# Kernel tuning notes

Measured on AMD Instinct MI355X. Metric: run time of the kernel, lower is better.

The kernel has to match this reference:

```python
import jax, jax.numpy as jnp
import numpy as np

N_NODES = 50000
N_EDGES = 600000
NODE_DIM = 128
HIDDEN = 128
LN_EPS = 1e-5


def setup_inputs() -> dict:
    key = jax.random.key(0)
    ks = jax.random.split(key, 12)
    x = jax.random.normal(ks[0], (N_NODES, NODE_DIM), dtype=jnp.float32)
    edge_index = jax.random.randint(ks[1], (2, N_EDGES), 0, N_NODES, dtype=jnp.int32)
    # GCNConv weights (glorot-ish scaling)
    W1 = jax.random.normal(ks[2], (NODE_DIM, HIDDEN), dtype=jnp.float32) / np.sqrt(NODE_DIM)
    b1 = jnp.zeros((HIDDEN,), jnp.float32)
    W2 = jax.random.normal(ks[3], (HIDDEN, HIDDEN), dtype=jnp.float32) / np.sqrt(HIDDEN)
    b2 = jnp.zeros((HIDDEN,), jnp.float32)
    g1 = jnp.ones((HIDDEN,), jnp.float32)
    beta1 = jnp.zeros((HIDDEN,), jnp.float32)
    g2 = jnp.ones((HIDDEN,), jnp.float32)
    beta2 = jnp.zeros((HIDDEN,), jnp.float32)
    return {"x": x, "edge_index": edge_index, "W1": W1, "b1": b1, "g1": g1,
            "beta1": beta1, "W2": W2, "b2": b2, "g2": g2, "beta2": beta2}


def _gcn_conv(x, src, dst, norm, W, b, n):
    # x' = sum_{j->i} norm_ji * (x_j @ W) + b   (self-loops already in src/dst)
    h = x @ W                                   # [N, H]
    msg = h[src] * norm[:, None]                # [E+N, H]
    out = jax.ops.segment_sum(msg, dst, num_segments=n)
    return out + b


def _layer_norm(x, gamma, beta):
    mu = jnp.mean(x, axis=-1, keepdims=True)
    var = jnp.mean((x - mu) ** 2, axis=-1, keepdims=True)
    return (x - mu) * jax.lax.rsqrt(var + LN_EPS) * gamma + beta


def reference(x, edge_index, W1, b1, g1, beta1, W2, b2, g2, beta2):
    n = x.shape[0]
    loop = jnp.arange(n, dtype=edge_index.dtype)
    src = jnp.concatenate([edge_index[0], loop])
    dst = jnp.concatenate([edge_index[1], loop])
    # symmetric normalization with self-loops (PyG GCNConv default)
    deg = jax.ops.segment_sum(jnp.ones_like(dst, dtype=x.dtype), dst, num_segments=n)
    dinv = jnp.where(deg > 0, jax.lax.rsqrt(jnp.maximum(deg, 1.0)), 0.0)
    norm = dinv[src] * dinv[dst]                # [E+N]

    h = _gcn_conv(x, src, dst, norm, W1, b1, n)
    h = _layer_norm(h, g1, beta1)
    h = jax.nn.relu(h)                          # relu between layers only
    h = _gcn_conv(h, src, dst, norm, W2, b2, n)
    h = _layer_norm(h, g2, beta2)
    return h
```

## Files before the change

### kernel.cpp

```cpp
#include <hip/hip_runtime.h>

#define DIM 128
#define LN_EPS 1e-5f

typedef __attribute__((ext_vector_type(8))) short bf16x8;
typedef __attribute__((ext_vector_type(4))) float f32x4;

static __device__ __forceinline__ unsigned short f2bf(float f) {
    unsigned int u = __builtin_bit_cast(unsigned int, f);
    u += 0x7fffu + ((u >> 16) & 1u);
    return (unsigned short)(u >> 16);
}
static __device__ __forceinline__ float bf2f_lo(unsigned int u) {
    return __builtin_bit_cast(float, u << 16);
}
static __device__ __forceinline__ float bf2f_hi(unsigned int u) {
    return __builtin_bit_cast(float, u & 0xffff0000u);
}

__global__ __launch_bounds__(256) void cvt_count_kernel(const float* __restrict__ X,
                                                        unsigned short* __restrict__ Y, int n4,
                                                        int nx4b,
                                                        const float* __restrict__ W1,
                                                        const float* __restrict__ W2,
                                                        unsigned short* __restrict__ Wt1,
                                                        unsigned short* __restrict__ Wt2,
                                                        const int* __restrict__ dst,
                                                        int* __restrict__ counts, int E) {
    int b = blockIdx.x;
    if (b < nx4b) {
        int i = b * 256 + threadIdx.x;
        if (i < n4) {
            float4 v = ((const float4*)X)[i];
            ushort4 o;
            o.x = f2bf(v.x); o.y = f2bf(v.y); o.z = f2bf(v.z); o.w = f2bf(v.w);
            ((ushort4*)Y)[i] = o;
        }
    } else if (b < nx4b + 128) {
        int elem = (b - nx4b) * 256 + threadIdx.x;
        int which = elem >> 14;
        int rest = elem & 16383;
        int c = rest >> 7;
        int k = rest & 127;
        const float* W = which ? W2 : W1;
        unsigned short* Wt = which ? Wt2 : Wt1;
        Wt[c * 128 + k] = f2bf(W[k * 128 + c]);
    } else {
        int e = (b - nx4b - 128) * 256 + threadIdx.x;
        if (e < E) atomicAdd(&counts[dst[e]], 1);
    }
}

__global__ __launch_bounds__(256) void scan1_kernel(const int* __restrict__ counts,
                                                    int* __restrict__ tmp,
                                                    int* __restrict__ bsums,
                                                    float* __restrict__ dinv, int n) {
    __shared__ int ts[256];
    int tid = threadIdx.x;
    int base = blockIdx.x * 1024 + tid * 4;
    int v[4];
#pragma unroll
    for (int j = 0; j < 4; ++j) {
        int i = base + j;
        v[j] = (i < n) ? counts[i] : 0;
        if (i < n) dinv[i] = rsqrtf((float)(v[j] + 1));
    }
    int s = v[0] + v[1] + v[2] + v[3];
    ts[tid] = s;
    __syncthreads();
    for (int off = 1; off < 256; off <<= 1) {
        int t2 = (tid >= off) ? ts[tid - off] : 0;
        __syncthreads();
        ts[tid] += t2;
        __syncthreads();
    }
    int excl = ts[tid] - s;
    int pre = excl;
#pragma unroll
    for (int j = 0; j < 4; ++j) {
        int i = base + j;
        if (i < n) tmp[i] = pre;
        pre += v[j];
    }
    if (tid == 255) bsums[blockIdx.x] = ts[255];
}

__global__ __launch_bounds__(256) void scan3_kernel(const int* __restrict__ tmp,
                                                    const int* __restrict__ bsums,
                                                    int* __restrict__ rowptr,
                                                    int* __restrict__ cursor,
                                                    int n, int E, int nb) {
    __shared__ int s_add;
    if (threadIdx.x < 64) {
        int lane = threadIdx.x;
        int v = (lane < nb) ? bsums[lane] : 0;
        int x = v;
#pragma unroll
        for (int off = 1; off < 64; off <<= 1) {
            int y = __shfl_up(x, off);
            if (lane >= off) x += y;
        }
        int excl = x - v;
        int mine = __builtin_amdgcn_readlane(excl, blockIdx.x);
        if (lane == 0) s_add = mine;
    }
    __syncthreads();
    int add = s_add;
    int base = blockIdx.x * 1024 + threadIdx.x * 4;
#pragma unroll
    for (int j = 0; j < 4; ++j) {
        int i = base + j;
        if (i < n) {
            int val = tmp[i] + add;
            rowptr[i] = val;
            cursor[i] = val;
        }
    }
    if (blockIdx.x == 0 && threadIdx.x == 0) rowptr[n] = E;
}

__global__ __launch_bounds__(256) void fill_kernel(const int* __restrict__ src,
                                                   const int* __restrict__ dst,
                                                   int* __restrict__ cursor,
                                                   unsigned short* __restrict__ colsrc, int E) {
    int e = blockIdx.x * 256 + threadIdx.x;
    if (e < E) {
        int p = atomicAdd(&cursor[dst[e]], 1);
        colsrc[p] = (unsigned short)src[e];
    }
}

__global__ __launch_bounds__(256) void gemm_mfma_kernel(const unsigned short* __restrict__ A,
                                                        const unsigned short* __restrict__ Bt,
                                                        const float* __restrict__ dinv,
                                                        unsigned short* __restrict__ H,
                                                        int n, int ntiles) {
    __shared__ unsigned short Wlds[128 * 136];

    for (int u = threadIdx.x; u < 2048; u += 256) {
        int row = u >> 4;
        int sub = u & 15;
        *(bf16x8*)&Wlds[row * 136 + sub * 8] = *(const bf16x8*)(Bt + row * 128 + sub * 8);
    }
    __syncthreads();

    int wid = threadIdx.x >> 6;
    int lane = threadIdx.x & 63;
    int tile = blockIdx.x * 4 + wid;
    if (tile >= ntiles) tile = ntiles - 1;
    int r0 = tile * 16;
    int mrow = lane & 15;
    int kgrp = lane >> 4;

    int arow_i = r0 + mrow;
    if (arow_i > n - 1) arow_i = n - 1;
    const unsigned short* arow = A + (size_t)arow_i * DIM + kgrp * 8;

    f32x4 acc[8];
#pragma unroll
    for (int t = 0; t < 8; ++t) acc[t] = (f32x4){0.f, 0.f, 0.f, 0.f};

#pragma unroll
    for (int kc = 0; kc < 4; ++kc) {
        bf16x8 af = *(const bf16x8*)(arow + kc * 32);
#pragma unroll
        for (int t = 0; t < 8; ++t) {
            bf16x8 bfv = *(const bf16x8*)&Wlds[(t * 16 + mrow) * 136 + kc * 32 + kgrp * 8];
            acc[t] = __builtin_amdgcn_mfma_f32_16x16x32_bf16(af, bfv, acc[t], 0, 0, 0);
        }
    }

    float dv[4];
#pragma unroll
    for (int reg = 0; reg < 4; ++reg) {
        int rr = r0 + kgrp * 4 + reg;
        dv[reg] = (rr < n) ? dinv[rr] : 0.f;
    }
#pragma unroll
    for (int t = 0; t < 8; ++t) {
#pragma unroll
        for (int reg = 0; reg < 4; ++reg) {
            int row = r0 + kgrp * 4 + reg;
            if (row < n) {
                int col = t * 16 + mrow;
                H[(size_t)row * DIM + col] = f2bf(acc[t][reg] * dv[reg]);
            }
        }
    }
}

__global__ __launch_bounds__(256) void gather_ln_kernel(const int* __restrict__ rowptr,
                                                        const unsigned short* __restrict__ colsrc,
                                                        const unsigned int* __restrict__ Hb,
                                                        const float* __restrict__ dinv,
                                                        const float* __restrict__ bias,
                                                        const float* __restrict__ gamma,
                                                        const float* __restrict__ beta,
                                                        unsigned int* __restrict__ out_bf,
                                                        float* __restrict__ out_f,
                                                        int n, int relu) {
    int wid = threadIdx.x >> 6;
    int lane = threadIdx.x & 63;
    int r = blockIdx.x * 4 + wid;
    if (r >= n) return;

    float di = dinv[r];
    float2 bb = ((const float2*)bias)[lane];
    float2 gg = ((const float2*)gamma)[lane];
    float2 be = ((const float2*)beta)[lane];

    unsigned int su = Hb[(size_t)r * 64 + lane];
    float ax = bf2f_lo(su), ay = bf2f_hi(su);

    int p = rowptr[r];
    int p1 = rowptr[r + 1];
    while (p < p1) {
        int cnt = p1 - p;
        if (cnt > 16) cnt = 16;
        int gi = p + lane;
        gi = gi < p1 ? gi : p1 - 1;
        int idxv = (int)colsrc[gi];

        unsigned int h[16];
#pragma unroll
        for (int j = 0; j < 16; ++j) {
            int s = __builtin_amdgcn_readlane(idxv, j);
            h[j] = Hb[(size_t)s * 64 + lane];
        }

#pragma unroll
        for (int j = 0; j < 16; ++j) {
            bool act = (j < cnt);
            ax += act ? bf2f_lo(h[j]) : 0.f;
            ay += act ? bf2f_hi(h[j]) : 0.f;
        }
        p += cnt;
    }

    float vx = ax * di + bb.x;
    float vy = ay * di + bb.y;

    float s1 = vx + vy;
    float s2 = vx * vx + vy * vy;
#pragma unroll
    for (int off = 32; off > 0; off >>= 1) {
        s1 += __shfl_xor(s1, off);
        s2 += __shfl_xor(s2, off);
    }
    float mu = s1 * (1.f / 128.f);
    float var = s2 * (1.f / 128.f) - mu * mu;
    float rstd = rsqrtf(var + LN_EPS);

    float ox = (vx - mu) * rstd * gg.x + be.x;
    float oy = (vy - mu) * rstd * gg.y + be.y;
    if (relu) {
        ox = fmaxf(ox, 0.f);
        oy = fmaxf(oy, 0.f);
    }
    if (out_bf) {
        unsigned int pk = (unsigned int)f2bf(ox) | ((unsigned int)f2bf(oy) << 16);
        out_bf[(size_t)r * 64 + lane] = pk;
    } else {
        ((float2*)out_f)[(size_t)r * 64 + lane] = make_float2(ox, oy);
    }
}

extern "C" void kernel_launch(void* const* d_in, const int* in_sizes, int n_in,
                              void* d_out, int out_size, void* d_ws, size_t ws_size,
                              hipStream_t stream) {
    const float* x   = (const float*)d_in[0];
    const int*   ei  = (const int*)d_in[1];
    const float* W1  = (const float*)d_in[2];
    const float* b1  = (const float*)d_in[3];
    const float* g1  = (const float*)d_in[4];
    const float* be1 = (const float*)d_in[5];
    const float* W2  = (const float*)d_in[6];
    const float* b2  = (const float*)d_in[7];
    const float* g2  = (const float*)d_in[8];
    const float* be2 = (const float*)d_in[9];

    int n = in_sizes[0] / DIM;
    int E = in_sizes[1] / 2;
    const int* src = ei;
    const int* dst = ei + E;

    char* wp = (char*)d_ws;
    auto alloc = [&](size_t bytes) {
        void* p = (void*)wp;
        wp += (bytes + 255) & ~(size_t)255;
        return p;
    };
    float*          dinv   = (float*)alloc((size_t)n * 4);
    int*            counts = (int*)alloc((size_t)n * 4);
    int*            tmp    = (int*)alloc((size_t)n * 4);
    int*            rowptr = (int*)alloc((size_t)(n + 1) * 4);
    int*            cursor = (int*)alloc((size_t)n * 4);
    int*            bsums  = (int*)alloc(64 * 4);
    unsigned short* colsrc = (unsigned short*)alloc((size_t)E * 2);
    unsigned short* xb     = (unsigned short*)alloc((size_t)n * DIM * 2);
    unsigned short* Wt1    = (unsigned short*)alloc(128 * 128 * 2);
    unsigned short* Wt2    = (unsigned short*)alloc(128 * 128 * 2);
    unsigned short* H      = (unsigned short*)alloc((size_t)n * DIM * 2);
    unsigned short* Y1     = (unsigned short*)alloc((size_t)n * DIM * 2);

    hipMemsetAsync(counts, 0, (size_t)n * 4, stream);

    int n4 = n * DIM / 4;
    int nx4b = (n4 + 255) / 256;
    int gE = (E + 255) / 256;
    cvt_count_kernel<<<nx4b + 128 + gE, 256, 0, stream>>>(x, xb, n4, nx4b, W1, W2, Wt1, Wt2,
                                                          dst, counts, E);

    int nb1 = (n + 1023) / 1024;
    scan1_kernel<<<nb1, 256, 0, stream>>>(counts, tmp, bsums, dinv, n);
    scan3_kernel<<<nb1, 256, 0, stream>>>(tmp, bsums, rowptr, cursor, n, E, nb1);
    fill_kernel<<<gE, 256, 0, stream>>>(src, dst, cursor, colsrc, E);

    int ntiles = (n + 15) / 16;
    int gG = (ntiles + 3) / 4;
    int gA = (n + 3) / 4;

    gemm_mfma_kernel<<<gG, 256, 0, stream>>>(xb, Wt1, dinv, H, n, ntiles);
    gather_ln_kernel<<<gA, 256, 0, stream>>>(rowptr, colsrc, (const unsigned int*)H, dinv,
                                             b1, g1, be1, (unsigned int*)Y1, nullptr, n, 1);

    gemm_mfma_kernel<<<gG, 256, 0, stream>>>(Y1, Wt2, dinv, H, n, ntiles);
    gather_ln_kernel<<<gA, 256, 0, stream>>>(rowptr, colsrc, (const unsigned int*)H, dinv,
                                             b2, g2, be2, nullptr, (float*)d_out, n, 0);
}
```

Before: 235.7 us.

## Split feature dim into four column slabs for cache-local gather, separate LayerNorm

The GEMM now writes H in a slab layout of four 32-column quarters, each stored contiguously. A new gather kernel aggregates one quarter per block, with the quarter chosen by block index, so each gather pass touches a 3.2 MB slab that can stay in L2 or LLC instead of the full 12.8 MB feature matrix. Aggregates are written as bf16 to a new buffer, and a separate LayerNorm kernel reads them back. This adds one kernel launch per layer, an extra round trip through memory, and an extra bf16 rounding of the aggregated sums before LayerNorm.

```diff
diff --git a/kernel.cpp b/kernel.cpp
--- a/kernel.cpp
+++ b/kernel.cpp
@@ -178,67 +178,90 @@
     }
 #pragma unroll
     for (int t = 0; t < 8; ++t) {
+        int q = t >> 1;
+        int c = (t & 1) * 16 + mrow;
 #pragma unroll
         for (int reg = 0; reg < 4; ++reg) {
             int row = r0 + kgrp * 4 + reg;
             if (row < n) {
-                int col = t * 16 + mrow;
-                H[(size_t)row * DIM + col] = f2bf(acc[t][reg] * dv[reg]);
+                H[((size_t)q * n + row) * 32 + c] = f2bf(acc[t][reg] * dv[reg]);
             }
         }
     }
 }
 
-__global__ __launch_bounds__(256) void gather_ln_kernel(const int* __restrict__ rowptr,
-                                                        const unsigned short* __restrict__ colsrc,
-                                                        const unsigned int* __restrict__ Hb,
-                                                        const float* __restrict__ dinv,
-                                                        const float* __restrict__ bias,
-                                                        const float* __restrict__ gamma,
-                                                        const float* __restrict__ beta,
-                                                        unsigned int* __restrict__ out_bf,
-                                                        float* __restrict__ out_f,
-                                                        int n, int relu) {
+__global__ __launch_bounds__(256) void gatherq_kernel(const int* __restrict__ rowptr,
+                                                      const unsigned short* __restrict__ colsrc,
+                                                      const unsigned int* __restrict__ H32,
+                                                      unsigned int* __restrict__ agg32,
+                                                      int n) {
+    int b = blockIdx.x;
+    int q = (b & 7) >> 1;
+    int i = (b >> 3) * 2 + (b & 1);
+    int wid = threadIdx.x >> 6;
+    int lane = threadIdx.x & 63;
+    int g = lane >> 4;
+    int t = lane & 15;
+    int r = i * 16 + wid * 4 + g;
+    if (r >= n) return;
+
+    const unsigned int* Hq = H32 + (size_t)q * n * 16;
+
+    unsigned int hv = Hq[(size_t)r * 16 + t];
+    float ax = bf2f_lo(hv), ay = bf2f_hi(hv);
+
+    int p = rowptr[r];
+    int p1 = rowptr[r + 1];
+    int gbase = g << 4;
+    while (p < p1) {
+        int cnt = p1 - p;
+        if (cnt > 16) cnt = 16;
+        int gi = p + t;
+        gi = gi < p1 ? gi : p1 - 1;
+        int idxv = (int)colsrc[gi];
+
+        unsigned int h[16];
+#pragma unroll
+        for (int j = 0; j < 16; ++j) {
+            int s = __shfl(idxv, gbase + j);
+            h[j] = Hq[(size_t)s * 16 + t];
+        }
+#pragma unroll
+        for (int j = 0; j < 16; ++j) {
+            bool act = (j < cnt);
+            ax += act ? bf2f_lo(h[j]) : 0.f;
+            ay += act ? bf2f_hi(h[j]) : 0.f;
+        }
+        p += cnt;
+    }
+
+    unsigned int pk = (unsigned int)f2bf(ax) | ((unsigned int)f2bf(ay) << 16);
+    __builtin_nontemporal_store(pk, &agg32[((size_t)q * n + r) * 16 + t]);
+}
+
+__global__ __launch_bounds__(256) void ln_kernel(const unsigned int* __restrict__ agg32,
+                                                 const float* __restrict__ dinv,
+                                                 const float* __restrict__ bias,
+                                                 const float* __restrict__ gamma,
+                                                 const float* __restrict__ beta,
+                                                 unsigned int* __restrict__ out_bf,
+                                                 float* __restrict__ out_f,
+                                                 int n, int relu) {
     int wid = threadIdx.x >> 6;
     int lane = threadIdx.x & 63;
     int r = blockIdx.x * 4 + wid;
     if (r >= n) return;
+    int q = lane >> 4;
+    int t = lane & 15;
 
     float di = dinv[r];
     float2 bb = ((const float2*)bias)[lane];
     float2 gg = ((const float2*)gamma)[lane];
     float2 be = ((const float2*)beta)[lane];
 
-    unsigned int su = Hb[(size_t)r * 64 + lane];
-    float ax = bf2f_lo(su), ay = bf2f_hi(su);
-
-    int p = rowptr[r];
-    int p1 = rowptr[r + 1];
-    while (p < p1) {
-        int cnt = p1 - p;
-        if (cnt > 16) cnt = 16;
-        int gi = p + lane;
-        gi = gi < p1 ? gi : p1 - 1;
-        int idxv = (int)colsrc[gi];
-
-        unsigned int h[16];
-#pragma unroll
-        for (int j = 0; j < 16; ++j) {
-            int s = __builtin_amdgcn_readlane(idxv, j);
-            h[j] = Hb[(size_t)s * 64 + lane];
-        }
-
-#pragma unroll
-        for (int j = 0; j < 16; ++j) {
-            bool act = (j < cnt);
-            ax += act ? bf2f_lo(h[j]) : 0.f;
-            ay += act ? bf2f_hi(h[j]) : 0.f;
-        }
-        p += cnt;
-    }
-
-    float vx = ax * di + bb.x;
-    float vy = ay * di + bb.y;
+    unsigned int av = __builtin_nontemporal_load(&agg32[((size_t)q * n + r) * 16 + t]);
+    float vx = bf2f_lo(av) * di + bb.x;
+    float vy = bf2f_hi(av) * di + bb.y;
 
     float s1 = vx + vy;
     float s2 = vx * vx + vy * vy;
@@ -301,6 +324,7 @@
     unsigned short* Wt1    = (unsigned short*)alloc(128 * 128 * 2);
     unsigned short* Wt2    = (unsigned short*)alloc(128 * 128 * 2);
     unsigned short* H      = (unsigned short*)alloc((size_t)n * DIM * 2);
+    unsigned short* Agg    = (unsigned short*)alloc((size_t)n * DIM * 2);
     unsigned short* Y1     = (unsigned short*)alloc((size_t)n * DIM * 2);
 
     hipMemsetAsync(counts, 0, (size_t)n * 4, stream);
@@ -318,13 +342,20 @@
 
     int ntiles = (n + 15) / 16;
     int gG = (ntiles + 3) / 4;
-    int gA = (n + 3) / 4;
+    int nodeblocks = (n + 15) / 16;
+    int nodeblocks2 = (nodeblocks + 1) & ~1;
+    int gQ = nodeblocks2 * 4;
+    int gL = (n + 3) / 4;
 
     gemm_mfma_kernel<<<gG, 256, 0, stream>>>(xb, Wt1, dinv, H, n, ntiles);
-    gather_ln_kernel<<<gA, 256, 0, stream>>>(rowptr, colsrc, (const unsigned int*)H, dinv,
-                                             b1, g1, be1, (unsigned int*)Y1, nullptr, n, 1);
+    gatherq_kernel<<<gQ, 256, 0, stream>>>(rowptr, colsrc, (const unsigned int*)H,
+                                           (unsigned int*)Agg, n);
+    ln_kernel<<<gL, 256, 0, stream>>>((const unsigned int*)Agg, dinv, b1, g1, be1,
+                                      (unsigned int*)Y1, nullptr, n, 1);
 
     gemm_mfma_kernel<<<gG, 256, 0, stream>>>(Y1, Wt2, dinv, H, n, ntiles);
-    gather_ln_kernel<<<gA, 256, 0, stream>>>(rowptr, colsrc, (const unsigned int*)H, dinv,
-                                             b2, g2, be2, nullptr, (float*)d_out, n, 0);
-}
+    gatherq_kernel<<<gQ, 256, 0, stream>>>(rowptr, colsrc, (const unsigned int*)H,
+                                           (unsigned int*)Agg, n);
+    ln_kernel<<<gL, 256, 0, stream>>>((const unsigned int*)Agg, dinv, b2, g2, be2,
+                                      nullptr, (float*)d_out, n, 0);
+}
```

New measurement: 262.2 us. +11.3%, slower.
